# Kernel tuning notes

Measured on AMD Instinct MI355X. Metric: run time of the kernel, lower is better.

The kernel has to match this reference:

```python
import jax, jax.numpy as jnp
import numpy as np

FEATURE_DIM = 256
HEADS = 8


def setup_inputs() -> dict:
    key = jax.random.key(0)
    ks = jax.random.split(key, 9)
    d, h = FEATURE_DIM, HEADS
    b, n = 4, 4096
    s_in = 1.0 / np.sqrt(d)
    s_out = 1.0 / np.sqrt(d * h)
    return {
        "x": jax.random.normal(ks[0], (b, n, d), dtype=jnp.float32),
        "Wq": jax.random.uniform(ks[1], (d, d * h), jnp.float32, -s_in, s_in),
        "bq": jax.random.uniform(ks[2], (d * h,), jnp.float32, -s_in, s_in),
        "Wk": jax.random.uniform(ks[3], (d, d * h), jnp.float32, -s_in, s_in),
        "bk": jax.random.uniform(ks[4], (d * h,), jnp.float32, -s_in, s_in),
        "Wv": jax.random.uniform(ks[5], (d, d * h), jnp.float32, -s_in, s_in),
        "bv": jax.random.uniform(ks[6], (d * h,), jnp.float32, -s_in, s_in),
        "Wo": jax.random.uniform(ks[7], (d * h, d), jnp.float32, -s_out, s_out),
        "bo": jax.random.uniform(ks[8], (d,), jnp.float32, -s_out, s_out),
    }


def reference(x, Wq, bq, Wk, bk, Wv, bv, Wo, bo):
    b, n, d = x.shape
    h = HEADS
    scale = d ** (-0.5)
    # projections: (b, n, h, d) -- note: NO head transpose, matching original
    q = (x @ Wq + bq).reshape(b, n, h, d)
    k = (x @ Wk + bk).reshape(b, n, h, d)
    v = (x @ Wv + bv).reshape(b, n, h, d)
    # attention is head-vs-head per token: (b, n, h, h)
    attn = jnp.einsum("bnhd,bngd->bnhg", q, k) * scale
    attn = jax.nn.softmax(attn, axis=-1)
    out = jnp.einsum("bnhg,bngd->bnhd", attn, v).reshape(b, n, h * d)
    return out @ Wo + bo
```

## Files before the change

### kernel.cpp

```cpp
#include <hip/hip_runtime.h>
#include <hip/hip_bf16.h>
#include <math.h>

typedef __bf16 bf16;
typedef __bf16 bf16x4 __attribute__((ext_vector_type(4)));
typedef __bf16 bf16x8 __attribute__((ext_vector_type(8)));
typedef float f32x4 __attribute__((ext_vector_type(4)));
typedef unsigned int u32;
typedef u32 __attribute__((address_space(1))) gu32;
typedef u32 __attribute__((address_space(3))) lu32;

#define TOK   16384
#define D_    256
#define HD    2048
#define QKVN  6144

#define GLDS16(g, l) __builtin_amdgcn_global_load_lds((gu32*)(g), (lu32*)(l), 16, 0, 0)
#define WAIT_VM(n) __builtin_amdgcn_s_waitcnt(0x0F70 | (n))

__device__ __forceinline__ void transpose_body(
    const void* __restrict__ src, bf16* __restrict__ dst, int R, int C,
    int tc, int tr, int f, float (*tile)[33])
{
    int lx = threadIdx.x & 31, ly = threadIdx.x >> 5;
    for (int i = 0; i < 4; i++) {
        int r = ly + i * 8;
        size_t idx = (size_t)(tr + r) * C + tc + lx;
        tile[r][lx] = f ? ((const float*)src)[idx] : (float)((const bf16*)src)[idx];
    }
    __syncthreads();
    for (int i = 0; i < 4; i++) {
        int r = ly + i * 8;
        dst[(size_t)(tc + r) * R + tr + lx] = (bf16)tile[lx][r];
    }
}

__global__ __launch_bounds__(256) void prep(
    const void* __restrict__ x,
    const void* __restrict__ Wq, const void* __restrict__ bq,
    const void* __restrict__ Wk, const void* __restrict__ bk,
    const void* __restrict__ Wv, const void* __restrict__ bv,
    const void* __restrict__ Wo, const void* __restrict__ bo,
    bf16* __restrict__ xb, bf16* __restrict__ WT, bf16* __restrict__ WoT,
    bf16* __restrict__ bqkv, bf16* __restrict__ bob)
{
    __shared__ float tile[32][33];
    __shared__ int sflag;
    int tid = threadIdx.x;
    if (tid == 0) sflag = 0;
    __syncthreads();
    {
        float v = fabsf((float)((const bf16*)x)[2 * tid]);
        if (!(v < 1e4f)) sflag = 1;
    }
    __syncthreads();
    int f = sflag;
    int b = blockIdx.x;

    if (b < 4096) {
        int i = b * 256 + tid;
        bf16x4 o;
        if (f) { f32x4 v = ((const f32x4*)x)[i]; for (int e = 0; e < 4; e++) o[e] = (bf16)v[e]; }
        else   { o = ((const bf16x4*)x)[i]; }
        ((bf16x4*)xb)[i] = o;
    } else if (b < 4121) {
        int i = (b - 4096) * 256 + tid;
        if (i < 6400) {
            const void* src; bf16* dst; int off;
            if (i < 2048)      { src = bq; dst = bqkv;        off = i; }
            else if (i < 4096) { src = bk; dst = bqkv + 2048; off = i - 2048; }
            else if (i < 6144) { src = bv; dst = bqkv + 4096; off = i - 4096; }
            else               { src = bo; dst = bob;         off = i - 6144; }
            float v = f ? ((const float*)src)[off] : (float)((const bf16*)src)[off];
            dst[off] = (bf16)v;
        }
        __syncthreads();
    } else if (b < 5657) {
        int idx = b - 4121;
        int tx = idx & 63, rest = idx >> 6;
        int ty = rest & 7, tz = rest >> 3;
        const void* src = (tz == 0) ? Wq : (tz == 1) ? Wk : Wv;
        bf16* dst = WT + (size_t)tz * 2048 * 256;
        transpose_body(src, dst, 256, 2048, tx * 32, ty * 32, f, tile);
    } else {
        int idx = b - 5657;
        int tx = idx & 7, ty = idx >> 3;
        transpose_body(Wo, WoT, 2048, 256, tx * 32, ty * 32, f, tile);
    }
}

__global__ __launch_bounds__(256) void proj_gemm(
    const bf16* __restrict__ X, const bf16* __restrict__ WT,
    const bf16* __restrict__ bqkv, bf16* __restrict__ qkv)
{
    __shared__ char smem[36864];
    bf16* As = (bf16*)smem;
    bf16* Bs = (bf16*)(smem + 16384);
    int m0 = blockIdx.y * 128, n0 = blockIdx.x * 128;
    int tid = threadIdx.x, wave = tid >> 6, lane = tid & 63;
    int wm = (wave >> 1) * 64, wn = (wave & 1) * 64;
    int mrow = lane & 15, quad = lane >> 4;
    int lrow8 = lane >> 3, lslot = lane & 7;

    f32x4 acc[4][4] = {};
    for (int k0 = 0; k0 < D_; k0 += 64) {
        __syncthreads();
        for (int i = 0; i < 4; i++) {
            int rbase = wave * 32 + i * 8;
            int row = rbase + lrow8;
            int gc = lslot ^ (row & 7);
            GLDS16(&X[(size_t)(m0 + row) * D_ + k0 + gc * 8], &As[rbase * 64]);
            GLDS16(&WT[(size_t)(n0 + row) * D_ + k0 + gc * 8], &Bs[rbase * 64]);
        }
        __syncthreads();
        for (int kk = 0; kk < 64; kk += 32) {
            int slot = (((kk >> 3) + quad) ^ (mrow & 7)) * 8;
            bf16x8 af[4], bfv[4];
            for (int mt = 0; mt < 4; mt++)
                af[mt] = *(const bf16x8*)&As[(wm + mt * 16 + mrow) * 64 + slot];
            for (int nt = 0; nt < 4; nt++)
                bfv[nt] = *(const bf16x8*)&Bs[(wn + nt * 16 + mrow) * 64 + slot];
            for (int mt = 0; mt < 4; mt++)
                for (int nt = 0; nt < 4; nt++)
                    acc[mt][nt] = __builtin_amdgcn_mfma_f32_16x16x32_bf16(
                        bfv[nt], af[mt], acc[mt][nt], 0, 0, 0);
        }
    }

    __syncthreads();
    bf16* ep = (bf16*)smem + wave * (64 * 72);
    for (int mt = 0; mt < 4; mt++) {
        for (int nt = 0; nt < 4; nt++) {
            int col = n0 + wn + nt * 16 + quad * 4;
            bf16x4 bb = *(const bf16x4*)&bqkv[col];
            bf16x4 o;
            for (int r = 0; r < 4; r++) o[r] = (bf16)(acc[mt][nt][r] + (float)bb[r]);
            *(bf16x4*)&ep[(mt * 16 + mrow) * 72 + nt * 16 + quad * 4] = o;
        }
    }
    __syncthreads();
    for (int i = 0; i < 8; i++) {
        int r = i * 8 + (lane >> 3);
        int cb = (lane & 7) * 8;
        bf16x8 val = *(const bf16x8*)&ep[r * 72 + cb];
        *(bf16x8*)&qkv[(size_t)(m0 + wm + r) * QKVN + n0 + wn + cb] = val;
    }
}

__global__ __launch_bounds__(256) void attn(bf16* __restrict__ qkv)
{
    __shared__ bf16 sh[4][6144];
    int wave = threadIdx.x >> 6, lane = threadIdx.x & 63;
    bf16* sq = sh[wave];
    int h = lane >> 3, g = lane & 7;
    int wid = blockIdx.x * 4 + wave;
    int start = (wid < 1024) ? wid * 6 : 6144 + (wid - 1024) * 5;
    int count = (wid < 1024) ? 6 : 5;

    for (int ti = 0; ti < count; ti++) {
        int t = start + ti;
        bf16* base = qkv + (size_t)t * QKVN;
        for (int i = 0; i < 12; i++) {
            int s = i * 64 + lane;
            int row = s >> 5, cs = s & 31;
            int gc = cs ^ (row & 7);
            GLDS16(base + row * 256 + gc * 8, (char*)sq + i * 1024);
        }
        WAIT_VM(4);

        const bf16* qrow = sq + h * 256;
        const bf16* krow = sq + (8 + g) * 256;
        float s0 = 0.f, s1 = 0.f, s2 = 0.f, s3 = 0.f;
        for (int c = 0; c < 32; c += 4) {
            bf16x8 a0 = *(const bf16x8*)&qrow[((c + 0) ^ h) * 8];
            bf16x8 b0 = *(const bf16x8*)&krow[((c + 0) ^ g) * 8];
            bf16x8 a1 = *(const bf16x8*)&qrow[((c + 1) ^ h) * 8];
            bf16x8 b1 = *(const bf16x8*)&krow[((c + 1) ^ g) * 8];
            bf16x8 a2 = *(const bf16x8*)&qrow[((c + 2) ^ h) * 8];
            bf16x8 b2 = *(const bf16x8*)&krow[((c + 2) ^ g) * 8];
            bf16x8 a3 = *(const bf16x8*)&qrow[((c + 3) ^ h) * 8];
            bf16x8 b3 = *(const bf16x8*)&krow[((c + 3) ^ g) * 8];
            for (int e = 0; e < 8; e++) {
                s0 += (float)a0[e] * (float)b0[e];
                s1 += (float)a1[e] * (float)b1[e];
                s2 += (float)a2[e] * (float)b2[e];
                s3 += (float)a3[e] * (float)b3[e];
            }
        }
        float s = ((s0 + s1) + (s2 + s3)) * 0.0625f;
        float m = s;
        for (int off = 1; off < 8; off <<= 1) m = fmaxf(m, __shfl_xor(m, off, 8));
        float p = __expf(s - m);
        float sum = p;
        for (int off = 1; off < 8; off <<= 1) sum += __shfl_xor(sum, off, 8);
        p /= sum;

        float pv[8];
        for (int g2 = 0; g2 < 8; g2++) pv[g2] = __shfl(p, h * 8 + g2, 64);

        WAIT_VM(0);

        float acc[4][8] = {};
        for (int g2 = 0; g2 < 8; g2++) {
            float pw = pv[g2];
            const bf16* vrow = sq + (16 + g2) * 256;
            for (int mm = 0; mm < 4; mm++) {
                bf16x8 v = *(const bf16x8*)&vrow[((g ^ g2) + 8 * mm) * 8];
                for (int e = 0; e < 8; e++) acc[mm][e] += pw * (float)v[e];
            }
        }
        bf16* obase = base + h * D_;
        for (int mm = 0; mm < 4; mm++) {
            bf16x8 o;
            for (int e = 0; e < 8; e++) o[e] = (bf16)acc[mm][e];
            *(bf16x8*)&obase[(g + 8 * mm) * 8] = o;
        }
    }
}

__global__ __launch_bounds__(256) void out_gemm(
    const bf16* __restrict__ qkv, const bf16* __restrict__ WoT,
    const bf16* __restrict__ bob, float* __restrict__ outp)
{
    __shared__ bf16 As[32 * 128];
    __shared__ bf16 Bs[128 * 128];
    int m0 = blockIdx.y * 32, n0 = blockIdx.x * 128;
    int tid = threadIdx.x, wave = tid >> 6, lane = tid & 63;
    int wm = (wave >> 1) * 16, wn = (wave & 1) * 64;
    int mrow = lane & 15, quad = lane >> 4;
    int lrow16 = lane >> 4, lslot16 = lane & 15;

    f32x4 acc[4] = {};
    for (int k0 = 0; k0 < HD; k0 += 128) {
        __syncthreads();
        for (int i = 0; i < 2; i++) {
            int rbase = wave * 8 + i * 4;
            int row = rbase + lrow16;
            int gc = lslot16 ^ (row & 7);
            GLDS16(&qkv[(size_t)(m0 + row) * QKVN + k0 + gc * 8], &As[rbase * 128]);
        }
        for (int i = 0; i < 8; i++) {
            int rbase = wave * 32 + i * 4;
            int row = rbase + lrow16;
            int gc = lslot16 ^ (row & 7);
            GLDS16(&WoT[(size_t)(n0 + row) * HD + k0 + gc * 8], &Bs[rbase * 128]);
        }
        __syncthreads();
        for (int kk = 0; kk < 128; kk += 32) {
            int slot = (((kk >> 3) + quad) ^ (mrow & 7)) * 8;
            bf16x8 af = *(const bf16x8*)&As[(wm + mrow) * 128 + slot];
            bf16x8 bfv[4];
            for (int nt = 0; nt < 4; nt++)
                bfv[nt] = *(const bf16x8*)&Bs[(wn + nt * 16 + mrow) * 128 + slot];
            for (int nt = 0; nt < 4; nt++)
                acc[nt] = __builtin_amdgcn_mfma_f32_16x16x32_bf16(
                    bfv[nt], af, acc[nt], 0, 0, 0);
        }
    }

    int row = m0 + wm + mrow;
    for (int nt = 0; nt < 4; nt++) {
        int col = n0 + wn + nt * 16 + quad * 4;
        bf16x4 bb = *(const bf16x4*)&bob[col];
        f32x4 o;
        for (int r = 0; r < 4; r++) o[r] = acc[nt][r] + (float)bb[r];
        *(f32x4*)&outp[(size_t)row * D_ + col] = o;
    }
}

extern "C" void kernel_launch(void* const* d_in, const int* in_sizes, int n_in,
                              void* d_out, int out_size, void* d_ws, size_t ws_size,
                              hipStream_t stream)
{
    const void* x  = d_in[0];
    const void* Wq = d_in[1];
    const void* bq = d_in[2];
    const void* Wk = d_in[3];
    const void* bk = d_in[4];
    const void* Wv = d_in[5];
    const void* bv = d_in[6];
    const void* Wo = d_in[7];
    const void* bo = d_in[8];
    float* out = (float*)d_out;

    char* ws = (char*)d_ws;
    bf16* qkv  = (bf16*)ws;
    bf16* WT   = (bf16*)(ws + 201326592);
    bf16* WoT  = (bf16*)(ws + 204472320);
    bf16* xb   = (bf16*)(ws + 205520896);
    bf16* bqkv = (bf16*)(ws + 213909504);
    bf16* bob  = (bf16*)(ws + 213921792);

    prep<<<6169, 256, 0, stream>>>(x, Wq, bq, Wk, bk, Wv, bv, Wo, bo,
                                   xb, WT, WoT, bqkv, bob);
    proj_gemm<<<dim3(48, 128), 256, 0, stream>>>(xb, WT, bqkv, qkv);
    attn<<<768, 256, 0, stream>>>(qkv);
    out_gemm<<<dim3(2, 512), 256, 0, stream>>>(qkv, WoT, bob, out);
}
```

Measured before the change: 240.1 us.

## Split attention into score kernel and fuse P·V into output GEMM

```diff
diff --git a/kernel.cpp b/kernel.cpp
--- a/kernel.cpp
+++ b/kernel.cpp
@@ -16,11 +16,10 @@
 #define QKVN  6144
 
 #define GLDS16(g, l) __builtin_amdgcn_global_load_lds((gu32*)(g), (lu32*)(l), 16, 0, 0)
-#define WAIT_VM(n) __builtin_amdgcn_s_waitcnt(0x0F70 | (n))
 
 __device__ __forceinline__ void transpose_body(
     const void* __restrict__ src, bf16* __restrict__ dst, int R, int C,
-    int tc, int tr, int f, float (*tile)[33])
+    int tc, int tr, int f, int perm, float (*tile)[33])
 {
     int lx = threadIdx.x & 31, ly = threadIdx.x >> 5;
     for (int i = 0; i < 4; i++) {
@@ -31,7 +30,11 @@
     __syncthreads();
     for (int i = 0; i < 4; i++) {
         int r = ly + i * 8;
-        dst[(size_t)(tc + r) * R + tr + lx] = (bf16)tile[lx][r];
+        int k = tr + lx;
+        size_t di = perm
+            ? (size_t)(tc + r) * R + (size_t)(k & 255) * 8 + (k >> 8)
+            : (size_t)(tc + r) * R + k;
+        dst[di] = (bf16)tile[lx][r];
     }
 }
 
@@ -81,11 +84,11 @@
         int ty = rest & 7, tz = rest >> 3;
         const void* src = (tz == 0) ? Wq : (tz == 1) ? Wk : Wv;
         bf16* dst = WT + (size_t)tz * 2048 * 256;
-        transpose_body(src, dst, 256, 2048, tx * 32, ty * 32, f, tile);
+        transpose_body(src, dst, 256, 2048, tx * 32, ty * 32, f, 0, tile);
     } else {
         int idx = b - 5657;
         int tx = idx & 7, ty = idx >> 3;
-        transpose_body(Wo, WoT, 2048, 256, tx * 32, ty * 32, f, tile);
+        transpose_body(Wo, WoT, 2048, 256, tx * 32, ty * 32, f, 1, tile);
     }
 }
 
@@ -147,39 +150,27 @@
     }
 }
 
-__global__ __launch_bounds__(256) void attn(bf16* __restrict__ qkv)
-{
-    __shared__ bf16 sh[4][6144];
+__global__ __launch_bounds__(256) void attn_score(
+    const bf16* __restrict__ qkv, float* __restrict__ P)
+{
     int wave = threadIdx.x >> 6, lane = threadIdx.x & 63;
-    bf16* sq = sh[wave];
     int h = lane >> 3, g = lane & 7;
     int wid = blockIdx.x * 4 + wave;
-    int start = (wid < 1024) ? wid * 6 : 6144 + (wid - 1024) * 5;
-    int count = (wid < 1024) ? 6 : 5;
-
-    for (int ti = 0; ti < count; ti++) {
-        int t = start + ti;
-        bf16* base = qkv + (size_t)t * QKVN;
-        for (int i = 0; i < 12; i++) {
-            int s = i * 64 + lane;
-            int row = s >> 5, cs = s & 31;
-            int gc = cs ^ (row & 7);
-            GLDS16(base + row * 256 + gc * 8, (char*)sq + i * 1024);
-        }
-        WAIT_VM(4);
-
-        const bf16* qrow = sq + h * 256;
-        const bf16* krow = sq + (8 + g) * 256;
+    for (int ti = 0; ti < 4; ti++) {
+        int t = wid * 4 + ti;
+        const bf16* qrow = qkv + (size_t)t * QKVN + h * 256;
+        const bf16* krow = qkv + (size_t)t * QKVN + 2048 + g * 256;
         float s0 = 0.f, s1 = 0.f, s2 = 0.f, s3 = 0.f;
+#pragma unroll
         for (int c = 0; c < 32; c += 4) {
-            bf16x8 a0 = *(const bf16x8*)&qrow[((c + 0) ^ h) * 8];
-            bf16x8 b0 = *(const bf16x8*)&krow[((c + 0) ^ g) * 8];
-            bf16x8 a1 = *(const bf16x8*)&qrow[((c + 1) ^ h) * 8];
-            bf16x8 b1 = *(const bf16x8*)&krow[((c + 1) ^ g) * 8];
-            bf16x8 a2 = *(const bf16x8*)&qrow[((c + 2) ^ h) * 8];
-            bf16x8 b2 = *(const bf16x8*)&krow[((c + 2) ^ g) * 8];
-            bf16x8 a3 = *(const bf16x8*)&qrow[((c + 3) ^ h) * 8];
-            bf16x8 b3 = *(const bf16x8*)&krow[((c + 3) ^ g) * 8];
+            bf16x8 a0 = *(const bf16x8*)&qrow[(c + 0) * 8];
+            bf16x8 b0 = *(const bf16x8*)&krow[(c + 0) * 8];
+            bf16x8 a1 = *(const bf16x8*)&qrow[(c + 1) * 8];
+            bf16x8 b1 = *(const bf16x8*)&krow[(c + 1) * 8];
+            bf16x8 a2 = *(const bf16x8*)&qrow[(c + 2) * 8];
+            bf16x8 b2 = *(const bf16x8*)&krow[(c + 2) * 8];
+            bf16x8 a3 = *(const bf16x8*)&qrow[(c + 3) * 8];
+            bf16x8 b3 = *(const bf16x8*)&krow[(c + 3) * 8];
             for (int e = 0; e < 8; e++) {
                 s0 += (float)a0[e] * (float)b0[e];
                 s1 += (float)a1[e] * (float)b1[e];
@@ -193,74 +184,86 @@
         float p = __expf(s - m);
         float sum = p;
         for (int off = 1; off < 8; off <<= 1) sum += __shfl_xor(sum, off, 8);
-        p /= sum;
-
-        float pv[8];
-        for (int g2 = 0; g2 < 8; g2++) pv[g2] = __shfl(p, h * 8 + g2, 64);
-
-        WAIT_VM(0);
-
-        float acc[4][8] = {};
-        for (int g2 = 0; g2 < 8; g2++) {
-            float pw = pv[g2];
-            const bf16* vrow = sq + (16 + g2) * 256;
-            for (int mm = 0; mm < 4; mm++) {
-                bf16x8 v = *(const bf16x8*)&vrow[((g ^ g2) + 8 * mm) * 8];
-                for (int e = 0; e < 8; e++) acc[mm][e] += pw * (float)v[e];
+        P[(size_t)t * 64 + lane] = p / sum;
+    }
+}
+
+__global__ __launch_bounds__(256) void out_fused(
+    const bf16* __restrict__ qkv, const bf16* __restrict__ WoT,
+    const float* __restrict__ P, const bf16* __restrict__ bob,
+    float* __restrict__ outp)
+{
+    __shared__ bf16 Bs[256 * 64];
+    __shared__ bf16 As[32 * 64];
+    __shared__ bf16 Vs[32 * 64];
+    int m0 = blockIdx.x * 32;
+    int tid = threadIdx.x, wave = tid >> 6, lane = tid & 63;
+    int wm = (wave >> 1) * 16, wn = (wave & 1) * 128;
+    int mrow = lane & 15, quad = lane >> 4;
+
+    int t = tid >> 3, dof = tid & 7, ts = t & 7;
+    int sl_t8 = lane >> 3, sl_g = lane & 7;
+
+    float Pv[64];
+    {
+        const float* pr = P + (size_t)(m0 + t) * 64;
+#pragma unroll
+        for (int j = 0; j < 16; j++) {
+            f32x4 v4 = *(const f32x4*)&pr[j * 4];
+            Pv[j * 4 + 0] = v4[0]; Pv[j * 4 + 1] = v4[1];
+            Pv[j * 4 + 2] = v4[2]; Pv[j * 4 + 3] = v4[3];
+        }
+    }
+
+    f32x4 acc[8] = {};
+    for (int c = 0; c < 32; c++) {
+        __syncthreads();
+        {
+            int tt = wave * 8 + sl_t8;
+            int gg = sl_g ^ (tt & 7);
+            GLDS16(&qkv[(size_t)(m0 + tt) * QKVN + 4096 + gg * 256 + c * 8],
+                   &Vs[wave * 512]);
+        }
+#pragma unroll
+        for (int i = 0; i < 8; i++) {
+            int n = wave * 64 + i * 8 + sl_t8;
+            int gc = sl_g ^ (n & 7);
+            GLDS16(&WoT[(size_t)n * HD + c * 64 + gc * 8],
+                   &Bs[(wave * 64 + i * 8) * 64]);
+        }
+        __syncthreads();
+        {
+            float vf[8];
+#pragma unroll
+            for (int g = 0; g < 8; g++)
+                vf[g] = (float)Vs[t * 64 + ((g ^ ts) << 3) + dof];
+            bf16x8 ao;
+#pragma unroll
+            for (int h = 0; h < 8; h++) {
+                float a = 0.f;
+#pragma unroll
+                for (int g = 0; g < 8; g++) a += Pv[h * 8 + g] * vf[g];
+                ao[h] = (bf16)a;
             }
-        }
-        bf16* obase = base + h * D_;
-        for (int mm = 0; mm < 4; mm++) {
-            bf16x8 o;
-            for (int e = 0; e < 8; e++) o[e] = (bf16)acc[mm][e];
-            *(bf16x8*)&obase[(g + 8 * mm) * 8] = o;
-        }
-    }
-}
-
-__global__ __launch_bounds__(256) void out_gemm(
-    const bf16* __restrict__ qkv, const bf16* __restrict__ WoT,
-    const bf16* __restrict__ bob, float* __restrict__ outp)
-{
-    __shared__ bf16 As[32 * 128];
-    __shared__ bf16 Bs[128 * 128];
-    int m0 = blockIdx.y * 32, n0 = blockIdx.x * 128;
-    int tid = threadIdx.x, wave = tid >> 6, lane = tid & 63;
-    int wm = (wave >> 1) * 16, wn = (wave & 1) * 64;
-    int mrow = lane & 15, quad = lane >> 4;
-    int lrow16 = lane >> 4, lslot16 = lane & 15;
-
-    f32x4 acc[4] = {};
-    for (int k0 = 0; k0 < HD; k0 += 128) {
-        __syncthreads();
-        for (int i = 0; i < 2; i++) {
-            int rbase = wave * 8 + i * 4;
-            int row = rbase + lrow16;
-            int gc = lslot16 ^ (row & 7);
-            GLDS16(&qkv[(size_t)(m0 + row) * QKVN + k0 + gc * 8], &As[rbase * 128]);
-        }
-        for (int i = 0; i < 8; i++) {
-            int rbase = wave * 32 + i * 4;
-            int row = rbase + lrow16;
-            int gc = lslot16 ^ (row & 7);
-            GLDS16(&WoT[(size_t)(n0 + row) * HD + k0 + gc * 8], &Bs[rbase * 128]);
-        }
-        __syncthreads();
-        for (int kk = 0; kk < 128; kk += 32) {
+            *(bf16x8*)&As[t * 64 + ((dof ^ ts) << 3)] = ao;
+        }
+        __syncthreads();
+#pragma unroll
+        for (int kk = 0; kk < 64; kk += 32) {
             int slot = (((kk >> 3) + quad) ^ (mrow & 7)) * 8;
-            bf16x8 af = *(const bf16x8*)&As[(wm + mrow) * 128 + slot];
-            bf16x8 bfv[4];
-            for (int nt = 0; nt < 4; nt++)
-                bfv[nt] = *(const bf16x8*)&Bs[(wn + nt * 16 + mrow) * 128 + slot];
-            for (int nt = 0; nt < 4; nt++)
-                acc[nt] = __builtin_amdgcn_mfma_f32_16x16x32_bf16(
-                    bfv[nt], af, acc[nt], 0, 0, 0);
+            bf16x8 af = *(const bf16x8*)&As[(wm + mrow) * 64 + slot];
+#pragma unroll
+            for (int nt = 0; nt < 8; nt++) {
+                bf16x8 bv = *(const bf16x8*)&Bs[(wn + nt * 16 + mrow) * 64 + slot];
+                acc[nt] = __builtin_amdgcn_mfma_f32_16x16x32_bf16(bv, af, acc[nt], 0, 0, 0);
+            }
         }
     }
 
     int row = m0 + wm + mrow;
-    for (int nt = 0; nt < 4; nt++) {
-        int col = n0 + wn + nt * 16 + quad * 4;
+#pragma unroll
+    for (int nt = 0; nt < 8; nt++) {
+        int col = wn + nt * 16 + quad * 4;
         bf16x4 bb = *(const bf16x4*)&bob[col];
         f32x4 o;
         for (int r = 0; r < 4; r++) o[r] = acc[nt][r] + (float)bb[r];
@@ -290,10 +293,11 @@
     bf16* xb   = (bf16*)(ws + 205520896);
     bf16* bqkv = (bf16*)(ws + 213909504);
     bf16* bob  = (bf16*)(ws + 213921792);
+    float* Pbuf = (float*)xb;
 
     prep<<<6169, 256, 0, stream>>>(x, Wq, bq, Wk, bk, Wv, bv, Wo, bo,
                                    xb, WT, WoT, bqkv, bob);
     proj_gemm<<<dim3(48, 128), 256, 0, stream>>>(xb, WT, bqkv, qkv);
-    attn<<<768, 256, 0, stream>>>(qkv);
-    out_gemm<<<dim3(2, 512), 256, 0, stream>>>(qkv, WoT, bob, out);
-}
+    attn_score<<<1024, 256, 0, stream>>>(qkv, Pbuf);
+    out_fused<<<512, 256, 0, stream>>>(qkv, WoT, Pbuf, bob, out);
+}
```

Result: slower. 285.4 us (+18.9%).
